# Kernel tuning notes

Measured on AMD Instinct MI355X. Metric: run time of the kernel, lower is better.

## Reference

```python
import jax, jax.numpy as jnp
import numpy as np

B, T, W = 4, 2048, 1024
K, G = 7, 8            # kernel_size, groups
Cg = W // G            # channels per group
SE_R = 16              # SE reduction ratio
LN_EPS = 1e-5


def setup_inputs() -> dict:
    key = jax.random.key(0)
    ks = jax.random.split(key, 8)
    h = jax.random.normal(ks[0], (B, T, W), jnp.float32)
    # mask: True = padding; valid prefix of random length per row
    lengths = jax.random.randint(ks[1], (B,), T // 2, T + 1)
    mask = jnp.arange(T)[None, :] >= lengths[:, None]
    s_w = np.float32(1.0 / np.sqrt(W))
    return dict(
        h=h,
        mask=mask,
        offset_w=jax.random.normal(ks[2], (W, K), jnp.float32) * 0.01,
        offset_b=jnp.zeros((K,), jnp.float32),
        conv_w=jax.random.normal(ks[3], (G, Cg, Cg, K), jnp.float32) * np.float32(1.0 / np.sqrt(Cg * K)),
        conv_b=jnp.zeros((W,), jnp.float32),
        ln_g=jnp.ones((W,), jnp.float32),
        ln_b=jnp.zeros((W,), jnp.float32),
        se_w1=jax.random.normal(ks[4], (W, W // SE_R), jnp.float32) * s_w,
        se_b1=jnp.zeros((W // SE_R,), jnp.float32),
        se_w2=jax.random.normal(ks[5], (W // SE_R, W), jnp.float32) * np.float32(1.0 / np.sqrt(W // SE_R)),
        se_b2=jnp.zeros((W,), jnp.float32),
        proj_w=jax.random.normal(ks[6], (W, 1), jnp.float32) * s_w,
        proj_b=jnp.zeros((1,), jnp.float32),
    )


def deform_conv1d(h, offset_w, offset_b, conv_w, conv_b):
    # h: [B,T,W]. Learned per-(position, tap) fractional offsets; linear interp gather;
    # grouped conv combine. conv_w: [G, out_per_group, in_per_group, K].
    Bn, Tn, Wn = h.shape
    pad = (K - 1) // 2
    offsets = h @ offset_w + offset_b                                   # [B,T,K]
    base = (jnp.arange(Tn, dtype=jnp.float32)[None, :, None]
            + (jnp.arange(K, dtype=jnp.float32) - pad)[None, None, :])  # [1,T,K]
    pos = jnp.clip(base + offsets, 0.0, Tn - 1.0)                       # [B,T,K]
    p0 = jnp.floor(pos).astype(jnp.int32)
    p1 = jnp.minimum(p0 + 1, Tn - 1)
    frac = (pos - p0.astype(jnp.float32))[..., None]                    # [B,T,K,1]
    gather = jax.vmap(lambda hb, ib: hb[ib])                            # [T,W],[T,K] -> [T,K,W]
    sampled = gather(h, p0) * (1.0 - frac) + gather(h, p1) * frac       # [B,T,K,W]
    sg = sampled.reshape(Bn, Tn, K, G, Cg)
    out = jnp.einsum('btkgc,gock->btgo', sg, conv_w).reshape(Bn, Tn, Wn)
    return out + conv_b


def layer_norm(x, g, b):
    mu = jnp.mean(x, axis=-1, keepdims=True)
    var = jnp.mean(jnp.square(x - mu), axis=-1, keepdims=True)
    return (x - mu) * jax.lax.rsqrt(var + LN_EPS) * g + b


def se_block(x, mask, w1, b1, w2, b2):
    valid = (~mask).astype(x.dtype)[..., None]                          # [B,T,1]
    lengths = jnp.clip(jnp.sum(valid, axis=1), 1.0)                     # [B,1]
    s = jnp.sum(x * valid, axis=1) / lengths                            # [B,W]
    gate = jax.nn.sigmoid(jax.nn.relu(s @ w1 + b1) @ w2 + b2)           # [B,W]
    return x * gate[:, None, :]


def reference(h, mask, offset_w, offset_b, conv_w, conv_b, ln_g, ln_b,
              se_w1, se_b1, se_w2, se_b2, proj_w, proj_b):
    x = layer_norm(deform_conv1d(h, offset_w, offset_b, conv_w, conv_b), ln_g, ln_b)
    x = se_block(x, mask, se_w1, se_b1, se_w2, se_b2)
    # dropout: identity in eval mode (p handled outside reference)
    valid = (~mask).astype(x.dtype)[..., None]
    x = x * valid                                                       # masked_fill(mask, 0)
    lengths = jnp.clip(jnp.sum(valid, axis=1), 1.0)                     # [B,1]
    pooled = jnp.sum(x, axis=1) / lengths                               # [B,W]
    return jnp.squeeze(pooled @ proj_w + proj_b, axis=-1)               # [B]
```

## Files before the change

### kernel.cpp

```cpp
#include <hip/hip_runtime.h>
#include <hip/hip_bf16.h>

#define Bdim 4
#define Tdim 2048
#define Wdim 1024
#define Kdim 7
#define Gdim 8
#define Cg   128
#define Hdim 64
#define TT   64

typedef __attribute__((ext_vector_type(8))) short short8v;
typedef __attribute__((ext_vector_type(4))) float float4v;

__device__ __forceinline__ short f2bf(float x) {
    union { float f; unsigned u; } v; v.f = x;
    unsigned r = v.u + 0x7fff + ((v.u >> 16) & 1);
    return (short)(r >> 16);
}

__device__ __forceinline__ unsigned pack2bf(float lo, float hi) {
    return __builtin_amdgcn_perm(__float_as_uint(hi) + 0x8000u,
                                 __float_as_uint(lo) + 0x8000u, 0x07060302u);
}

__device__ __forceinline__ short8v lerp_pack(uint4 a, uint4 b, float f) {
    union { uint4 u; short8v s; } r;
    const unsigned* pa = (const unsigned*)&a;
    const unsigned* pb = (const unsigned*)&b;
    unsigned* pr = (unsigned*)&r.u;
#pragma unroll
    for (int d = 0; d < 4; d++) {
        float alo = __uint_as_float(pa[d] << 16);
        float ahi = __uint_as_float(pa[d] & 0xffff0000u);
        float blo = __uint_as_float(pb[d] << 16);
        float bhi = __uint_as_float(pb[d] & 0xffff0000u);
        float rlo = alo + f * (blo - alo);
        float rhi = ahi + f * (bhi - ahi);
        pr[d] = pack2bf(rlo, rhi);
    }
    return r.s;
}

__global__ __launch_bounds__(256) void k_pre(const float* __restrict__ conv_w,
                                             short* __restrict__ Wtb,
                                             const float* __restrict__ h,
                                             const float* __restrict__ offset_w,
                                             const float* __restrict__ offset_b,
                                             float* __restrict__ pos,
                                             ushort* __restrict__ h16,
                                             float* __restrict__ rowstat) {
    int tid = threadIdx.x;
    if (blockIdx.x < 448) {
        if (blockIdx.x < 64) rowstat[blockIdx.x * 256 + tid] = 0.f;
        int i = blockIdx.x * 256 + tid;
        int cb = i & 15;
        int o = (i >> 4) & 127;
        int gk = i >> 11;
        int k = gk % Kdim, g = gk / Kdim;
        const float* src = conv_w + ((size_t)(g * Cg + o) * Cg + cb * 8) * Kdim + k;
        short8v pk;
#pragma unroll
        for (int j = 0; j < 8; j++) pk[j] = f2bf(src[(size_t)j * Kdim]);
        short8v* Wtb8 = (short8v*)Wtb;
        Wtb8[(size_t)gk * 2048 + o * 16 + cb] = pk;
        return;
    }
    __shared__ float ow_t[Kdim * Wdim];
    int lane = tid & 63, wv = tid >> 6;
    for (int u = tid; u < Kdim * Wdim; u += 256) {
        int c = u / Kdim, k = u - c * Kdim;
        ow_t[k * Wdim + c] = offset_w[u];
    }
    __syncthreads();
    int base = (blockIdx.x - 448) * 16 + wv * 4;
#pragma unroll 1
    for (int i = 0; i < 4; i++) {
        int bt = base + i;
        int t = bt & (Tdim - 1);
        const float* hrow = h + (size_t)bt * Wdim;
        float acc[Kdim];
#pragma unroll
        for (int k = 0; k < Kdim; k++) acc[k] = 0.f;
#pragma unroll
        for (int j = 0; j < 4; j++) {
            int c = lane * 4 + j * 256;
            float4 hv = *(const float4*)(hrow + c);
#pragma unroll
            for (int k = 0; k < Kdim; k++) {
                float4 wk = *(const float4*)&ow_t[k * Wdim + c];
                acc[k] += hv.x * wk.x + hv.y * wk.y + hv.z * wk.z + hv.w * wk.w;
            }
            ushort4 hp;
            hp.x = (ushort)f2bf(hv.x); hp.y = (ushort)f2bf(hv.y);
            hp.z = (ushort)f2bf(hv.z); hp.w = (ushort)f2bf(hv.w);
            *(ushort4*)(h16 + (size_t)bt * Wdim + c) = hp;
        }
#pragma unroll
        for (int k = 0; k < Kdim; k++) {
#pragma unroll
            for (int m = 32; m > 0; m >>= 1) acc[k] += __shfl_xor(acc[k], m);
        }
        if (lane == 0) {
#pragma unroll
            for (int k = 0; k < Kdim; k++) {
                float o = acc[k] + offset_b[k];
                float bs = (float)t + (float)(k - 3);
                float p = fminf(fmaxf(bs + o, 0.f), (float)(Tdim - 1));
                pos[bt * Kdim + k] = p;
            }
        }
    }
}

__global__ __launch_bounds__(256, 4) void k_conv(const ushort* __restrict__ h16,
                                                 const short* __restrict__ Wtb,
                                                 const float* __restrict__ conv_b,
                                                 const float* __restrict__ pos,
                                                 ushort* __restrict__ y16,
                                                 float* __restrict__ rowstat) {
    __shared__ short8v sA8[2][TT * 16];
    __shared__ float posl[TT * 8];

    int blk = blockIdx.x;
    int g  = blk & 7;
    int tc = (blk >> 3) & 31;
    int b  = blk >> 8;
    int t0 = tc * TT;
    int tid = threadIdx.x;
    int lane = tid & 63, wv = tid >> 6;
    int r15 = lane & 15, q = lane >> 4;

    const ushort* hb = h16 + (size_t)(b * Tdim) * Wdim + g * Cg;
    const short8v* WtbV = (const short8v*)Wtb + (size_t)(g * Kdim) * 2048;

    int scb = tid & 15;
    int sr0 = tid >> 4;

    {
        int base = (b * Tdim + t0) * Kdim;
        for (int u = tid; u < TT * Kdim; u += 256) {
            int r = u / 7, kk = u - r * 7;
            posl[r * 8 + kk] = pos[base + u];
        }
    }
    __syncthreads();

    float4v acc[4][2];
#pragma unroll
    for (int tt = 0; tt < 4; tt++)
#pragma unroll
        for (int n = 0; n < 2; n++) acc[tt][n] = (float4v){0.f, 0.f, 0.f, 0.f};

    float fr[4];
    uint4 glo[4], ghi[4];
#pragma unroll
    for (int i = 0; i < 4; i++) {
        int r = sr0 + i * 16;
        float p = posl[r * 8 + 0];
        int p0 = (int)p;
        fr[i] = p - (float)p0;
        int p1 = min(p0 + 1, Tdim - 1);
        glo[i] = *(const uint4*)(hb + (size_t)p0 * Wdim + scb * 8);
        ghi[i] = *(const uint4*)(hb + (size_t)p1 * Wdim + scb * 8);
    }

#pragma unroll 1
    for (int k = 0; k < Kdim; k++) {
        short8v bfr[8];
#pragma unroll
        for (int n = 0; n < 2; n++)
#pragma unroll
            for (int kk = 0; kk < 4; kk++)
                bfr[n * 4 + kk] =
                    WtbV[(size_t)k * 2048 + (wv * 32 + n * 16 + r15) * 16 + kk * 4 + q];
        short8v* buf = sA8[k & 1];
#pragma unroll
        for (int i = 0; i < 4; i++) {
            int r = sr0 + i * 16;
            buf[r * 16 + (scb ^ (r & 7))] = lerp_pack(glo[i], ghi[i], fr[i]);
        }
        __syncthreads();
        if (k < Kdim - 1) {
#pragma unroll
            for (int i = 0; i < 4; i++) {
                int r = sr0 + i * 16;
                float p = posl[r * 8 + k + 1];
                int p0 = (int)p;
                fr[i] = p - (float)p0;
                int p1 = min(p0 + 1, Tdim - 1);
                glo[i] = *(const uint4*)(hb + (size_t)p0 * Wdim + scb * 8);
                ghi[i] = *(const uint4*)(hb + (size_t)p1 * Wdim + scb * 8);
            }
        }
#pragma unroll
        for (int tt = 0; tt < 4; tt++) {
            int r = tt * 16 + r15;
            short8v af[4];
#pragma unroll
            for (int kk = 0; kk < 4; kk++)
                af[kk] = buf[r * 16 + ((kk * 4 + q) ^ (r & 7))];
#pragma unroll
            for (int kk = 0; kk < 4; kk++) {
#pragma unroll
                for (int n = 0; n < 2; n++)
                    acc[tt][n] = __builtin_amdgcn_mfma_f32_16x16x32_bf16(
                        af[kk], bfr[n * 4 + kk], acc[tt][n], 0, 0, 0);
            }
        }
    }
    __syncthreads();
    float* ep = (float*)sA8;
#pragma unroll
    for (int n = 0; n < 2; n++) {
        int colb = wv * 32 + n * 16 + r15;
        float bias = conv_b[g * Cg + colb];
#pragma unroll
        for (int tt = 0; tt < 4; tt++)
#pragma unroll
            for (int j = 0; j < 4; j++) {
                int row = tt * 16 + q * 4 + j;
                ep[row * 128 + (colb ^ ((row & 7) << 2))] = acc[tt][n][j] + bias;
            }
    }
    __syncthreads();
    int row = tid >> 2, c0 = (tid & 3) * 32;
    int sw = (row & 7) << 2;
    ushort* yp = y16 + (size_t)(b * Tdim + t0 + row) * Wdim + g * Cg + c0;
    float s_part = 0.f, q_part = 0.f;
#pragma unroll
    for (int s = 0; s < 4; s++) {
        float4 va = *(const float4*)&ep[row * 128 + ((c0 + s * 8) ^ sw)];
        float4 vb = *(const float4*)&ep[row * 128 + ((c0 + s * 8 + 4) ^ sw)];
        s_part += va.x + va.y + va.z + va.w + vb.x + vb.y + vb.z + vb.w;
        q_part += va.x * va.x + va.y * va.y + va.z * va.z + va.w * va.w
                + vb.x * vb.x + vb.y * vb.y + vb.z * vb.z + vb.w * vb.w;
        uint4 o;
        o.x = pack2bf(va.x, va.y);
        o.y = pack2bf(va.z, va.w);
        o.z = pack2bf(vb.x, vb.y);
        o.w = pack2bf(vb.z, vb.w);
        *(uint4*)(yp + s * 8) = o;
    }
    s_part += __shfl_xor(s_part, 1); s_part += __shfl_xor(s_part, 2);
    q_part += __shfl_xor(q_part, 1); q_part += __shfl_xor(q_part, 2);
    if ((tid & 3) == 0) {
        atomicAdd(&rowstat[(b * Tdim + t0 + row) * 2 + 0], s_part);
        atomicAdd(&rowstat[(b * Tdim + t0 + row) * 2 + 1], q_part);
    }
}

__global__ __launch_bounds__(256) void k_lnpool(const ushort* __restrict__ y16,
                                                const int* __restrict__ mask,
                                                const float* __restrict__ rowstat,
                                                float* __restrict__ part) {
    int blk = blockIdx.x;
    int b = blk >> 6, ch = blk & 63;
    int tid = threadIdx.x;
    int c0 = tid * 4;
    float a0 = 0.f, a1 = 0.f, a2 = 0.f, a3 = 0.f;
#pragma unroll 4
    for (int i = 0; i < 32; i++) {
        int t = ch * 32 + i;
        if (mask[b * Tdim + t]) continue;
        float2 st = *(const float2*)(rowstat + (b * Tdim + t) * 2);
        float mu = st.x * (1.f / Wdim);
        float inv = rsqrtf(st.y * (1.f / Wdim) - mu * mu + 1e-5f);
        uint2 u = *(const uint2*)(y16 + (size_t)(b * Tdim + t) * Wdim + c0);
        float v0 = __uint_as_float(u.x << 16);
        float v1 = __uint_as_float(u.x & 0xffff0000u);
        float v2 = __uint_as_float(u.y << 16);
        float v3 = __uint_as_float(u.y & 0xffff0000u);
        a0 += (v0 - mu) * inv; a1 += (v1 - mu) * inv;
        a2 += (v2 - mu) * inv; a3 += (v3 - mu) * inv;
    }
    *(float4*)(part + (size_t)blk * Wdim + c0) = (float4){a0, a1, a2, a3};
}

__global__ __launch_bounds__(256) void k_sefinal(const float* __restrict__ part,
                                                 const int* __restrict__ mask,
                                                 const float* __restrict__ ln_g,
                                                 const float* __restrict__ ln_b,
                                                 const float* __restrict__ w1,
                                                 const float* __restrict__ b1,
                                                 const float* __restrict__ w2,
                                                 const float* __restrict__ b2,
                                                 const float* __restrict__ projw,
                                                 const float* __restrict__ projb,
                                                 float* __restrict__ out) {
    int b = blockIdx.x, tid = threadIdx.x;
    __shared__ float s[Wdim];
    __shared__ float hred[4][Hdim];
    __shared__ float hid[Hdim];
    __shared__ float rbuf[4];
    __shared__ float sLinv;
    int lane = tid & 63, wv = tid >> 6;

    int cnt = 0;
    for (int t = tid; t < Tdim; t += 256) cnt += (mask[b * Tdim + t] ? 0 : 1);
    float fc = (float)cnt;
#pragma unroll
    for (int off = 32; off > 0; off >>= 1) fc += __shfl_down(fc, off);
    if (lane == 0) rbuf[wv] = fc;
    __syncthreads();
    if (tid == 0) {
        float L = rbuf[0] + rbuf[1] + rbuf[2] + rbuf[3];
        sLinv = 1.f / fmaxf(L, 1.f);
    }
    __syncthreads();
    float Linv = sLinv;

    int w4 = tid * 4;
    float4 a = {0.f, 0.f, 0.f, 0.f};
    for (int chh = 0; chh < 64; chh++) {
        float4 p = *(const float4*)(part + (size_t)(b * 64 + chh) * Wdim + w4);
        a.x += p.x; a.y += p.y; a.z += p.z; a.w += p.w;
    }
    float4 gg = *(const float4*)(ln_g + w4);
    float4 bb = *(const float4*)(ln_b + w4);
    s[w4 + 0] = gg.x * (a.x * Linv) + bb.x;
    s[w4 + 1] = gg.y * (a.y * Linv) + bb.y;
    s[w4 + 2] = gg.z * (a.z * Linv) + bb.z;
    s[w4 + 3] = gg.w * (a.w * Linv) + bb.w;
    __syncthreads();

    int j = tid & 63, p = tid >> 6;
    float ha = 0.f;
    for (int w = p * 256; w < (p + 1) * 256; ++w) ha += s[w] * w1[(size_t)w * Hdim + j];
    hred[p][j] = ha;
    __syncthreads();
    if (tid < Hdim)
        hid[tid] = fmaxf(hred[0][tid] + hred[1][tid] + hred[2][tid] + hred[3][tid] + b1[tid], 0.f);
    __syncthreads();

    float part2 = 0.f;
    for (int w = tid; w < Wdim; w += 256) {
        float ga = b2[w];
#pragma unroll 8
        for (int j2 = 0; j2 < Hdim; j2++) ga += hid[j2] * w2[(size_t)j2 * Wdim + w];
        float gate = 1.f / (1.f + expf(-ga));
        part2 += s[w] * gate * projw[w];
    }
#pragma unroll
    for (int off = 32; off > 0; off >>= 1) part2 += __shfl_down(part2, off);
    __syncthreads();
    if (lane == 0) rbuf[wv] = part2;
    __syncthreads();
    if (tid == 0) out[b] = rbuf[0] + rbuf[1] + rbuf[2] + rbuf[3] + projb[0];
}

extern "C" void kernel_launch(void* const* d_in, const int* in_sizes, int n_in,
                              void* d_out, int out_size, void* d_ws, size_t ws_size,
                              hipStream_t stream) {
    const float* h        = (const float*)d_in[0];
    const int*   mask     = (const int*)d_in[1];
    const float* offset_w = (const float*)d_in[2];
    const float* offset_b = (const float*)d_in[3];
    const float* conv_w   = (const float*)d_in[4];
    const float* conv_b   = (const float*)d_in[5];
    const float* ln_g     = (const float*)d_in[6];
    const float* ln_b     = (const float*)d_in[7];
    const float* se_w1    = (const float*)d_in[8];
    const float* se_b1    = (const float*)d_in[9];
    const float* se_w2    = (const float*)d_in[10];
    const float* se_b2    = (const float*)d_in[11];
    const float* proj_w   = (const float*)d_in[12];
    const float* proj_b   = (const float*)d_in[13];
    float* out = (float*)d_out;

    char* wsb = (char*)d_ws;
    float*  pos     = (float*)(wsb);
    ushort* h16     = (ushort*)(wsb + 229376);
    short*  Wtb     = (short*)(wsb + 17006592);
    ushort* y16     = (ushort*)(wsb + 18841600);
    float*  rowstat = (float*)(wsb + 35618816);
    float*  part    = (float*)(wsb + 35684352);

    k_pre<<<dim3(448 + 512), dim3(256), 0, stream>>>(conv_w, Wtb, h, offset_w,
                                                     offset_b, pos, h16, rowstat);
    k_conv<<<dim3(Bdim * (Tdim / TT) * Gdim), dim3(256), 0, stream>>>(h16, Wtb, conv_b,
                                                                      pos, y16, rowstat);
    k_lnpool<<<dim3(Bdim * 64), dim3(256), 0, stream>>>(y16, mask, rowstat, part);
    k_sefinal<<<dim3(Bdim), dim3(256), 0, stream>>>(part, mask, ln_g, ln_b,
                                                    se_w1, se_b1, se_w2, se_b2,
                                                    proj_w, proj_b, out);
}
```

Baseline: 102.0 us.

## Fuse LN-pool and SE-final kernels via last-block atomic counter; halve k_pre row blocks

After: 123.9 us. 1.21x slower.

```diff
diff --git a/kernel.cpp b/kernel.cpp
--- a/kernel.cpp
+++ b/kernel.cpp
@@ -49,9 +49,11 @@
                                              const float* __restrict__ offset_b,
                                              float* __restrict__ pos,
                                              ushort* __restrict__ h16,
-                                             float* __restrict__ rowstat) {
+                                             float* __restrict__ rowstat,
+                                             unsigned* __restrict__ cnt) {
     int tid = threadIdx.x;
     if (blockIdx.x < 448) {
+        if (blockIdx.x == 0 && tid < Bdim) cnt[tid] = 0u;
         if (blockIdx.x < 64) rowstat[blockIdx.x * 256 + tid] = 0.f;
         int i = blockIdx.x * 256 + tid;
         int cb = i & 15;
@@ -73,9 +75,9 @@
         ow_t[k * Wdim + c] = offset_w[u];
     }
     __syncthreads();
-    int base = (blockIdx.x - 448) * 16 + wv * 4;
+    int base = (blockIdx.x - 448) * 32 + wv * 8;
 #pragma unroll 1
-    for (int i = 0; i < 4; i++) {
+    for (int i = 0; i < 8; i++) {
         int bt = base + i;
         int t = bt & (Tdim - 1);
         const float* hrow = h + (size_t)bt * Wdim;
@@ -250,10 +252,20 @@
     }
 }
 
-__global__ __launch_bounds__(256) void k_lnpool(const ushort* __restrict__ y16,
-                                                const int* __restrict__ mask,
-                                                const float* __restrict__ rowstat,
-                                                float* __restrict__ part) {
+__global__ __launch_bounds__(256) void k_lnse(const ushort* __restrict__ y16,
+                                              const int* __restrict__ mask,
+                                              const float* __restrict__ rowstat,
+                                              float* __restrict__ part,
+                                              unsigned* __restrict__ cnt,
+                                              const float* __restrict__ ln_g,
+                                              const float* __restrict__ ln_b,
+                                              const float* __restrict__ w1,
+                                              const float* __restrict__ b1,
+                                              const float* __restrict__ w2,
+                                              const float* __restrict__ b2,
+                                              const float* __restrict__ projw,
+                                              const float* __restrict__ projb,
+                                              float* __restrict__ out) {
     int blk = blockIdx.x;
     int b = blk >> 6, ch = blk & 63;
     int tid = threadIdx.x;
@@ -275,20 +287,14 @@
         a2 += (v2 - mu) * inv; a3 += (v3 - mu) * inv;
     }
     *(float4*)(part + (size_t)blk * Wdim + c0) = (float4){a0, a1, a2, a3};
-}
-
-__global__ __launch_bounds__(256) void k_sefinal(const float* __restrict__ part,
-                                                 const int* __restrict__ mask,
-                                                 const float* __restrict__ ln_g,
-                                                 const float* __restrict__ ln_b,
-                                                 const float* __restrict__ w1,
-                                                 const float* __restrict__ b1,
-                                                 const float* __restrict__ w2,
-                                                 const float* __restrict__ b2,
-                                                 const float* __restrict__ projw,
-                                                 const float* __restrict__ projb,
-                                                 float* __restrict__ out) {
-    int b = blockIdx.x, tid = threadIdx.x;
+
+    __threadfence();
+    __shared__ unsigned old_s;
+    if (tid == 0) old_s = atomicAdd(&cnt[b], 1u);
+    __syncthreads();
+    if (old_s != 63u) return;
+    __threadfence();
+
     __shared__ float s[Wdim];
     __shared__ float hred[4][Hdim];
     __shared__ float hid[Hdim];
@@ -296,9 +302,9 @@
     __shared__ float sLinv;
     int lane = tid & 63, wv = tid >> 6;
 
-    int cnt = 0;
-    for (int t = tid; t < Tdim; t += 256) cnt += (mask[b * Tdim + t] ? 0 : 1);
-    float fc = (float)cnt;
+    int cnt2 = 0;
+    for (int t = tid; t < Tdim; t += 256) cnt2 += (mask[b * Tdim + t] ? 0 : 1);
+    float fc = (float)cnt2;
 #pragma unroll
     for (int off = 32; off > 0; off >>= 1) fc += __shfl_down(fc, off);
     if (lane == 0) rbuf[wv] = fc;
@@ -369,19 +375,19 @@
     float* out = (float*)d_out;
 
     char* wsb = (char*)d_ws;
-    float*  pos     = (float*)(wsb);
-    ushort* h16     = (ushort*)(wsb + 229376);
-    short*  Wtb     = (short*)(wsb + 17006592);
-    ushort* y16     = (ushort*)(wsb + 18841600);
-    float*  rowstat = (float*)(wsb + 35618816);
-    float*  part    = (float*)(wsb + 35684352);
-
-    k_pre<<<dim3(448 + 512), dim3(256), 0, stream>>>(conv_w, Wtb, h, offset_w,
-                                                     offset_b, pos, h16, rowstat);
+    float*    pos     = (float*)(wsb);
+    ushort*   h16     = (ushort*)(wsb + 229376);
+    short*    Wtb     = (short*)(wsb + 17006592);
+    ushort*   y16     = (ushort*)(wsb + 18841600);
+    float*    rowstat = (float*)(wsb + 35618816);
+    float*    part    = (float*)(wsb + 35684352);
+    unsigned* cnt     = (unsigned*)(wsb + 36732928);
+
+    k_pre<<<dim3(448 + 256), dim3(256), 0, stream>>>(conv_w, Wtb, h, offset_w,
+                                                     offset_b, pos, h16, rowstat, cnt);
     k_conv<<<dim3(Bdim * (Tdim / TT) * Gdim), dim3(256), 0, stream>>>(h16, Wtb, conv_b,
                                                                       pos, y16, rowstat);
-    k_lnpool<<<dim3(Bdim * 64), dim3(256), 0, stream>>>(y16, mask, rowstat, part);
-    k_sefinal<<<dim3(Bdim), dim3(256), 0, stream>>>(part, mask, ln_g, ln_b,
-                                                    se_w1, se_b1, se_w2, se_b2,
-                                                    proj_w, proj_b, out);
-}
+    k_lnse<<<dim3(Bdim * 64), dim3(256), 0, stream>>>(y16, mask, rowstat, part, cnt,
+                                                      ln_g, ln_b, se_w1, se_b1, se_w2, se_b2,
+                                                      proj_w, proj_b, out);
+}
```
